# Kernel optimization log

Measured on AMD Instinct MI355X. Metric: run time of the kernel, lower is better.

## Reference

```python
import jax, jax.numpy as jnp
import numpy as np

P, C, D = 65536, 64, 256

def setup_inputs() -> dict:
    key = jax.random.key(0)
    k1, k2, k3, k4 = jax.random.split(key, 4)
    return {
        "protos1": jax.random.normal(k1, (P, D), dtype=jnp.float32),
        "protos2": jax.random.normal(k2, (P, D), dtype=jnp.float32),
        "W": jax.random.normal(k3, (D, D), dtype=jnp.float32) / np.float32(np.sqrt(D)),
        "b": jax.random.normal(k4, (D,), dtype=jnp.float32),
        "num_classes": C,
    }

def _pairwise_dist(x, y):
    # x: (C, n, D), y: (C, m, D) -> squared-euclidean-style dists (C, n, m)
    xs = jnp.sum(x * x, axis=-1)[:, :, None]
    ys = jnp.sum(y * y, axis=-1)[:, None, :]
    return xs + ys - 2.0 * jnp.einsum('cid,cjd->cij', x, y)

def reference(protos1, protos2, W, b, num_classes):
    nc = int(num_classes)
    d = protos1.shape[-1]
    # prototypes[c::num_classes] for all c at once: (P,D) -> (P//C, C, D) -> (C, P//C, D)
    p1 = protos1.reshape(-1, nc, d).transpose(1, 0, 2)
    p2 = protos2.reshape(-1, nc, d).transpose(1, 0, 2)
    # transition: nn.Linear -> x @ W.T + b ; inverse: (x - b) @ inv(W.T)
    p2_inv = (p2 - b) @ jnp.linalg.inv(W.T)
    p1_fwd = p1 @ W.T + b
    a = _pairwise_dist(p1, p2_inv)          # (C, n, n)
    bb = _pairwise_dist(p2, p1_fwd)         # (C, n, n)
    proto_losses_source = jnp.mean(jnp.min(a, axis=2), axis=1)   # (C,)
    proto_losses_target = jnp.mean(jnp.min(bb, axis=2), axis=1)  # (C,)
    return jnp.stack([proto_losses_source, proto_losses_target])  # (2, C)
```

## Files before the change

### kernel.cpp

```cpp
#include <hip/hip_runtime.h>

#define D 256
#define NC 64

using u16 = unsigned short;
using u32 = unsigned int;

typedef __attribute__((ext_vector_type(8))) short bfv8;
typedef __attribute__((ext_vector_type(4))) float f32x4;
typedef __attribute__((ext_vector_type(2))) int v2i;

__device__ __forceinline__ float bf2f(u32 u) {
  union { u32 i; float f; } v; v.i = u << 16; return v.f;
}
__device__ __forceinline__ u16 f2bf(float f) {
  union { float f; u32 i; } v; v.f = f;
  u32 x = v.i;
  return (u16)((x + 0x7FFFu + ((x >> 16) & 1u)) >> 16);
}
__device__ __forceinline__ u32 pk2(float a, float b) {
  return (u32)f2bf(a) | ((u32)f2bf(b) << 16);
}
__device__ __forceinline__ size_t cmrow(int g) {
  return (size_t)(((g & 63) << 10) | (g >> 6));
}

__device__ __forceinline__ void gload_lds16(const void* src, void* dst) {
  __builtin_amdgcn_global_load_lds(
      (const __attribute__((address_space(1))) void*)src,
      (__attribute__((address_space(3))) void*)dst, 16, 0, 0);
}

#define GJ_LDS 71168
#define DISTP_LDS 135680

__device__ void gj_body(const float* __restrict__ W, float* __restrict__ IW,
                        char* smem) {
  float (*Ml)[20]    = (float(*)[20])smem;
  float (*Arow)[256] = (float(*)[256])(smem + 20480);
  float (*G)[256]    = (float(*)[256])(smem + 36864);
  u16*  Gfrag        = (u16*)(smem + 53248);
  float (*Pinv)[20]  = (float(*)[20])(smem + 69888);
  const int t = threadIdx.x, w = t >> 6, l = t & 63;
  const int lj = l & 15, lh = l >> 4;
  const int r0 = 16 * w;
  const bool lo32 = (l < 32);

  f32x4 x[16];
#pragma unroll
  for (int ct = 0; ct < 16; ++ct)
#pragma unroll
    for (int reg = 0; reg < 4; ++reg)
      x[ct][reg] = W[(size_t)(r0 + 4 * lh + reg) * D + 16 * ct + lj];

  for (int s = 0; s < 16; ++s) {
#pragma unroll
    for (int ct = 0; ct < 16; ++ct)
      if (ct == s)
#pragma unroll
        for (int reg = 0; reg < 4; ++reg)
          Ml[r0 + 4 * lh + reg][lj] = x[ct][reg];
    if (w == s) {
#pragma unroll
      for (int ct = 0; ct < 16; ++ct)
#pragma unroll
        for (int reg = 0; reg < 4; ++reg)
          Arow[4 * lh + reg][16 * ct + lj] = x[ct][reg];
    }
    bfv8 afr;
    {
      const int row = r0 + lj;
      float4 f0 = *(const float4*)&Ml[row][8 * (lh & 1)];
      float4 f1 = *(const float4*)&Ml[row][8 * (lh & 1) + 4];
      const float fv[8] = {f0.x, f0.y, f0.z, f0.w, f1.x, f1.y, f1.z, f1.w};
      union { bfv8 v; u16 e[8]; } A;
      if (lh < 2) {
#pragma unroll
        for (int e = 0; e < 8; ++e) A.e[e] = f2bf(-fv[e]);
      } else {
#pragma unroll
        for (int e = 0; e < 8; ++e) {
          const float hi = bf2f(f2bf(fv[e]));
          A.e[e] = f2bf(-(fv[e] - hi));
        }
      }
      afr = A.v;
    }
    __syncthreads();
    if (t < 16) {
      float p[16];
      {
        float4 rr0 = *(const float4*)&Ml[16 * s + t][0];
        float4 rr1 = *(const float4*)&Ml[16 * s + t][4];
        float4 rr2 = *(const float4*)&Ml[16 * s + t][8];
        float4 rr3 = *(const float4*)&Ml[16 * s + t][12];
        p[0] = rr0.x; p[1] = rr0.y; p[2] = rr0.z; p[3] = rr0.w;
        p[4] = rr1.x; p[5] = rr1.y; p[6] = rr1.z; p[7] = rr1.w;
        p[8] = rr2.x; p[9] = rr2.y; p[10] = rr2.z; p[11] = rr2.w;
        p[12] = rr3.x; p[13] = rr3.y; p[14] = rr3.z; p[15] = rr3.w;
      }
#pragma unroll
      for (int pp = 0; pp < 16; ++pp) {
        float u[16];
#pragma unroll
        for (int j = 0; j < 16; ++j)
          u[j] = __int_as_float(__builtin_amdgcn_readlane(__float_as_int(p[j]), pp));
        const float pv = u[pp];
        const float d = 1.0f / pv;
        if (t == pp) {
#pragma unroll
          for (int j = 0; j < 16; ++j) p[j] = u[j] * d;
          p[pp] = d;
        } else {
          const float md = p[pp] * d;
          u[pp] = pv + 1.0f;
#pragma unroll
          for (int j = 0; j < 16; ++j) p[j] = fmaf(-md, u[j], p[j]);
        }
      }
#pragma unroll
      for (int j = 0; j < 16; ++j) Pinv[t][j] = p[j];
    }
    __syncthreads();
    {
      const bool inC = ((l >> 2) == s);
      const int co = (l & 3) << 2;
      const int gct = l >> 2;
      const int kk = w;
      float4 g = make_float4(0.f, 0.f, 0.f, 0.f);
#pragma unroll
      for (int q = 0; q < 16; ++q) {
        const float pv = Pinv[kk][q];
        const float4 av = *(const float4*)&Arow[q][4 * l];
        g.x = fmaf(pv, av.x, g.x); g.y = fmaf(pv, av.y, g.y);
        g.z = fmaf(pv, av.z, g.z); g.w = fmaf(pv, av.w, g.w);
      }
      if (inC) {
        g.x = Pinv[kk][co + 0] + (kk == co + 0 ? 1.f : 0.f);
        g.y = Pinv[kk][co + 1] + (kk == co + 1 ? 1.f : 0.f);
        g.z = Pinv[kk][co + 2] + (kk == co + 2 ? 1.f : 0.f);
        g.w = Pinv[kk][co + 3] + (kk == co + 3 ? 1.f : 0.f);
      }
      *(float4*)&G[kk][4 * l] = g;
      const int e0 = kk & 7;
      const int lbase = 16 * (kk >> 3);
      const float gv[4] = {g.x, g.y, g.z, g.w};
#pragma unroll
      for (int cc = 0; cc < 4; ++cc) {
        const int cl = 4 * (l & 3) + cc;
        const u16 hi = f2bf(gv[cc]);
        const u16 lo = f2bf(gv[cc] - bf2f(hi));
        Gfrag[gct * 520 + (lbase + cl) * 8 + e0] = hi;
        Gfrag[gct * 520 + (32 + lbase + cl) * 8 + e0] = lo;
      }
    }
    __syncthreads();
    if (w != s) {
#pragma unroll
      for (int ct = 0; ct < 16; ++ct) {
        union { bfv8 v; uint4 u; } B1, B2;
        B1.v = *(const bfv8*)&Gfrag[ct * 520 + l * 8];
#if __has_builtin(__builtin_amdgcn_permlane32_swap)
        {
          v2i r;
          r = __builtin_amdgcn_permlane32_swap((int)B1.u.x, (int)B1.u.x, false, false);
          B2.u.x = lo32 ? (u32)r.y : (u32)r.x;
          r = __builtin_amdgcn_permlane32_swap((int)B1.u.y, (int)B1.u.y, false, false);
          B2.u.y = lo32 ? (u32)r.y : (u32)r.x;
          r = __builtin_amdgcn_permlane32_swap((int)B1.u.z, (int)B1.u.z, false, false);
          B2.u.z = lo32 ? (u32)r.y : (u32)r.x;
          r = __builtin_amdgcn_permlane32_swap((int)B1.u.w, (int)B1.u.w, false, false);
          B2.u.w = lo32 ? (u32)r.y : (u32)r.x;
        }
#else
        B2.v = *(const bfv8*)&Gfrag[ct * 520 + (l ^ 32) * 8];
#endif
        x[ct] = __builtin_amdgcn_mfma_f32_16x16x32_bf16(afr, B1.v, x[ct], 0, 0, 0);
        x[ct] = __builtin_amdgcn_mfma_f32_16x16x32_bf16(afr, B2.v, x[ct], 0, 0, 0);
      }
    } else {
#pragma unroll
      for (int ct = 0; ct < 16; ++ct) {
        if (ct == s) {
#pragma unroll
          for (int reg = 0; reg < 4; ++reg)
            x[ct][reg] = Pinv[4 * lh + reg][lj];
        } else {
#pragma unroll
          for (int reg = 0; reg < 4; ++reg)
            x[ct][reg] = G[4 * lh + reg][16 * ct + lj];
        }
      }
    }
    __syncthreads();
  }
#pragma unroll
  for (int ct = 0; ct < 16; ++ct)
#pragma unroll
    for (int reg = 0; reg < 4; ++reg)
      IW[(size_t)(r0 + 4 * lh + reg) * D + 16 * ct + lj] = x[ct][reg];
}

__device__ void convnorm_role(const float* __restrict__ P, u16* __restrict__ Pb,
                              float* __restrict__ nrm, int blk) {
  const int tx = threadIdx.x;
  const int r = tx >> 2, q = tx & 3;
  const int g = blk * 256 + r;
  const float* src = P + (size_t)g * D + q * 64;
  u16* dst = Pb + cmrow(g) * D + q * 64;
  float ss = 0.f;
#pragma unroll
  for (int g4 = 0; g4 < 8; ++g4) {
    float4 v0 = *(const float4*)(src + g4 * 8);
    float4 v1 = *(const float4*)(src + g4 * 8 + 4);
    ss = fmaf(v0.x, v0.x, fmaf(v0.y, v0.y, fmaf(v0.z, v0.z, fmaf(v0.w, v0.w, ss))));
    ss = fmaf(v1.x, v1.x, fmaf(v1.y, v1.y, fmaf(v1.z, v1.z, fmaf(v1.w, v1.w, ss))));
    uint4 w4;
    w4.x = pk2(v0.x, v0.y); w4.y = pk2(v0.z, v0.w);
    w4.z = pk2(v1.x, v1.y); w4.w = pk2(v1.z, v1.w);
    *(uint4*)(dst + g4 * 8) = w4;
  }
  ss += __shfl_xor(ss, 1, 64);
  ss += __shfl_xor(ss, 2, 64);
  if (q == 0) nrm[cmrow(g)] = ss;
}

template <int MODE>
__device__ void distp_body(const float* __restrict__ Pj,
                           const u16* __restrict__ Brows,
                           const float* __restrict__ biasv,
                           const u16* __restrict__ Pib,
                           const float* __restrict__ nB,
                           float* __restrict__ pmind, int bid, char* smem) {
  const int lb = (bid & 7) * 64 + (bid >> 3);
  const int c = lb >> 3, jt = lb & 7;
  const int tx = threadIdx.x, ww = tx >> 6, l = tx & 63;
  const int mw = ww >> 3, nw = ww & 7, l4 = l >> 4, lm = l & 15;
  char* Ab = smem;
  char* Bb = smem + 65536;
  float* nfpart = (float*)(smem + 131072);
  float* minbuf = (float*)(smem + 131072);
  float* nAb = (float*)(smem + 135168);

  auto issue_chunk = [&](int buf, int ch) {
#pragma unroll
    for (int u = 0; u < 2; ++u) {
      const int chunk = ww * 2 + u, ks = chunk >> 2, n = chunk & 3;
      const u16* src = Pib + ((size_t)(c << 10) + ch * 64 + n * 16 + lm) * D
                       + ks * 32 + l4 * 8;
      gload_lds16(src, Bb + buf * 32768 + chunk * 1024);
    }
  };

  bfv8 bfr[2][8];
#pragma unroll
  for (int nf2 = 0; nf2 < 2; ++nf2)
#pragma unroll
    for (int ks = 0; ks < 8; ++ks)
      bfr[nf2][ks] = *(const bfv8*)(Brows +
          (size_t)(nw * 32 + nf2 * 16 + lm) * D + ks * 32 + l4 * 8);
  {
    const int r = tx >> 3, sg = tx & 7;
    const float* arow = Pj + ((size_t)(jt * 128 + r) * NC + c) * D + sg * 32;
#pragma unroll
    for (int g2 = 0; g2 < 4; ++g2) {
      float4 v0 = *(const float4*)(arow + g2 * 8);
      float4 v1 = *(const float4*)(arow + g2 * 8 + 4);
      uint4 w4;
      w4.x = pk2(v0.x, v0.y); w4.y = pk2(v0.z, v0.w);
      w4.z = pk2(v1.x, v1.y); w4.w = pk2(v1.z, v1.w);
      *(uint4*)(Ab + (sg * 8 + (r >> 4)) * 1024 + ((r & 15) + g2 * 16) * 16) = w4;
    }
  }
  __syncthreads();
  const bfv8* A8 = (const bfv8*)Ab;
  f32x4 acc[4][2];
#pragma unroll
  for (int mf = 0; mf < 4; ++mf) {
    acc[mf][0] = f32x4{0.f, 0.f, 0.f, 0.f};
    acc[mf][1] = f32x4{0.f, 0.f, 0.f, 0.f};
  }
#pragma unroll
  for (int ks = 0; ks < 8; ++ks)
#pragma unroll
    for (int mf = 0; mf < 4; ++mf) {
      bfv8 a = A8[(ks * 8 + mw * 4 + mf) * 64 + l];
      acc[mf][0] = __builtin_amdgcn_mfma_f32_16x16x32_bf16(a, bfr[0][ks], acc[mf][0], 0, 0, 0);
      acc[mf][1] = __builtin_amdgcn_mfma_f32_16x16x32_bf16(a, bfr[1][ks], acc[mf][1], 0, 0, 0);
    }
  float bias[2];
  if (MODE == 0) {
#pragma unroll
    for (int nf2 = 0; nf2 < 2; ++nf2)
      bias[nf2] = biasv[nw * 32 + nf2 * 16 + lm];
  } else {
#pragma unroll
    for (int nf2 = 0; nf2 < 2; ++nf2) {
      float pd = 0.f;
#pragma unroll
      for (int ks = 0; ks < 8; ++ks) {
        float4 b0 = *(const float4*)(biasv + ks * 32 + l4 * 8);
        float4 b1 = *(const float4*)(biasv + ks * 32 + l4 * 8 + 4);
        pd = fmaf(b0.x, bf2f((u16)bfr[nf2][ks][0]), pd);
        pd = fmaf(b0.y, bf2f((u16)bfr[nf2][ks][1]), pd);
        pd = fmaf(b0.z, bf2f((u16)bfr[nf2][ks][2]), pd);
        pd = fmaf(b0.w, bf2f((u16)bfr[nf2][ks][3]), pd);
        pd = fmaf(b1.x, bf2f((u16)bfr[nf2][ks][4]), pd);
        pd = fmaf(b1.y, bf2f((u16)bfr[nf2][ks][5]), pd);
        pd = fmaf(b1.z, bf2f((u16)bfr[nf2][ks][6]), pd);
        pd = fmaf(b1.w, bf2f((u16)bfr[nf2][ks][7]), pd);
      }
      pd += __shfl_xor(pd, 16, 64);
      pd += __shfl_xor(pd, 32, 64);
      bias[nf2] = -pd;
    }
  }
  __syncthreads();
  issue_chunk(0, 0);
  u16* tile = (u16*)Ab;
#pragma unroll
  for (int mf = 0; mf < 4; ++mf)
#pragma unroll
    for (int rr = 0; rr < 4; ++rr) {
      const int j = mw * 64 + mf * 16 + l4 * 4 + rr;
      float v2 = 0.f;
#pragma unroll
      for (int nf2 = 0; nf2 < 2; ++nf2) {
        const float v = acc[mf][nf2][rr] + bias[nf2];
        const u16 hv = f2bf(v);
        tile[(((nw * 8 + mw * 4 + mf) << 6) + ((nf2 * 2 + (lm >> 3)) << 4)
              + l4 * 4 + rr) * 8 + (lm & 7)] = hv;
        const float vr = bf2f(hv);
        v2 = fmaf(vr, vr, v2);
      }
      v2 += __shfl_xor(v2, 1, 64);
      v2 += __shfl_xor(v2, 2, 64);
      v2 += __shfl_xor(v2, 4, 64);
      v2 += __shfl_xor(v2, 8, 64);
      if (lm == 0) nfpart[nw * 128 + j] = v2;
    }
  __syncthreads();
  if (tx < 128) {
    float s = 0.f;
#pragma unroll
    for (int q = 0; q < 8; ++q) s += nfpart[q * 128 + tx];
    nAb[tx] = s;
  }
  __syncthreads();
  const int jw = ww >> 1, iw = ww & 1;
  const float* nBc = nB + (c << 10);
  const size_t obase = (size_t)(c * 8 + jt) * 1024;
  for (int ch = 0; ch < 16; ++ch) {
    if (ch < 15) issue_chunk((ch + 1) & 1, ch + 1);
    const bfv8* B8 = (const bfv8*)(Bb + (ch & 1) * 32768);
    f32x4 a2[2];
    a2[0] = f32x4{0.f, 0.f, 0.f, 0.f};
    a2[1] = f32x4{0.f, 0.f, 0.f, 0.f};
#pragma unroll
    for (int ks = 0; ks < 8; ++ks) {
      bfv8 a = A8[(ks * 8 + jw) * 64 + l];
#pragma unroll
      for (int t = 0; t < 2; ++t) {
        bfv8 b = B8[(ks * 4 + iw * 2 + t) * 64 + l];
        a2[t] = __builtin_amdgcn_mfma_f32_16x16x32_bf16(a, b, a2[t], 0, 0, 0);
      }
    }
#pragma unroll
    for (int t = 0; t < 2; ++t) {
      const int ig = iw * 2 + t;
      const float nb = nBc[ch * 64 + ig * 16 + lm];
      float mm = 3.0e38f;
#pragma unroll
      for (int rr = 0; rr < 4; ++rr) {
        const int j = jw * 16 + l4 * 4 + rr;
        const float dd = nb + nAb[j] - 2.0f * a2[t][rr];
        mm = fminf(mm, dd);
      }
      mm = fminf(mm, __shfl_xor(mm, 16, 64));
      mm = fminf(mm, __shfl_xor(mm, 32, 64));
      if (l4 == 0) minbuf[jw * 64 + ig * 16 + lm] = mm;
    }
    __syncthreads();
    if (tx < 64) {
      float m = minbuf[tx];
#pragma unroll
      for (int q = 1; q < 8; ++q) m = fminf(m, minbuf[q * 64 + tx]);
      pmind[obase + ch * 64 + tx] = m;
    }
    __syncthreads();
  }
}

__global__ __launch_bounds__(1024, 1) void k0_kernel(
    const float* __restrict__ p2, u16* __restrict__ p2b,
    float* __restrict__ n2, const float* __restrict__ W,
    u16* __restrict__ Wb) {
  if (blockIdx.x < 256) {
    convnorm_role(p2, p2b, n2, blockIdx.x);
  } else {
    const int t = threadIdx.x;
#pragma unroll
    for (int k = 0; k < 64; ++k) Wb[k * 1024 + t] = f2bf(W[k * 1024 + t]);
  }
}

__global__ __launch_bounds__(1024, 1) void k1_kernel(
    const float* __restrict__ p1, const float* __restrict__ W,
    const u16* __restrict__ Wb, const float* __restrict__ bv,
    const u16* __restrict__ p2b, const float* __restrict__ n2,
    float* __restrict__ pmin1, float* __restrict__ IWa,
    u16* __restrict__ p1b, float* __restrict__ n1) {
  extern __shared__ char smem[];
  const int b = blockIdx.x;
  if (b == 0) {
    gj_body(W, IWa, smem);
  } else if (b <= 512) {
    distp_body<0>(p1, Wb, bv, p2b, n2, pmin1, b - 1, smem);
  } else {
    convnorm_role(p1, p1b, n1, b - 513);
  }
}

__global__ __launch_bounds__(256) void nr_residual(const float* __restrict__ W,
                                                   const float* __restrict__ X,
                                                   float* __restrict__ R) {
  __shared__ float wrow[D];
  const int i = blockIdx.x, j = threadIdx.x;
  wrow[j] = W[i * D + j];
  __syncthreads();
  float acc = 0.f;
#pragma unroll 8
  for (int k = 0; k < D; ++k) acc = fmaf(wrow[k], X[k * D + j], acc);
  R[i * D + j] = (i == j ? 2.0f : 0.0f) - acc;
}

__global__ __launch_bounds__(256) void nr_mult_bf16(const float* __restrict__ X,
                                                    const float* __restrict__ R,
                                                    u16* __restrict__ Yb) {
  __shared__ float xrow[D];
  const int i = blockIdx.x, j = threadIdx.x;
  xrow[j] = X[i * D + j];
  __syncthreads();
  float acc = 0.f;
#pragma unroll 8
  for (int k = 0; k < D; ++k) acc = fmaf(xrow[k], R[k * D + j], acc);
  Yb[i * D + j] = f2bf(acc);
}

__global__ __launch_bounds__(1024, 1) void k3_kernel(
    const float* __restrict__ p2, const u16* __restrict__ IWb,
    const float* __restrict__ bv, const u16* __restrict__ p1b,
    const float* __restrict__ n1, float* __restrict__ pmin0) {
  extern __shared__ char smem[];
  distp_body<1>(p2, IWb, bv, p1b, n1, pmin0, blockIdx.x, smem);
}

__global__ __launch_bounds__(256) void final_kernel(const float* __restrict__ pmin,
                                                    float* __restrict__ out) {
  __shared__ float ws4[4];
  const int dc = blockIdx.x, tx = threadIdx.x;
  const float* base = pmin + (size_t)dc * 8192;
  float s = 0.f;
#pragma unroll
  for (int t = 0; t < 4; ++t) {
    const int i = t * 256 + tx;
    float m = base[i];
#pragma unroll
    for (int j = 1; j < 8; ++j) m = fminf(m, base[j * 1024 + i]);
    s += m;
  }
#pragma unroll
  for (int off = 32; off; off >>= 1) s += __shfl_xor(s, off, 64);
  if ((tx & 63) == 0) ws4[tx >> 6] = s;
  __syncthreads();
  if (tx == 0)
    out[dc] = (ws4[0] + ws4[1] + ws4[2] + ws4[3]) * (1.0f / 1024.0f);
}

extern "C" void kernel_launch(void* const* d_in, const int* in_sizes, int n_in,
                              void* d_out, int out_size, void* d_ws, size_t ws_size,
                              hipStream_t stream) {
  const float* p1 = (const float*)d_in[0];
  const float* p2 = (const float*)d_in[1];
  const float* W  = (const float*)d_in[2];
  const float* bv = (const float*)d_in[3];
  float* out = (float*)d_out;
  char* ws = (char*)d_ws;
  float* n1  = (float*)(ws);
  float* n2  = (float*)(ws + (256 << 10));
  u16* Wb    = (u16*)(ws + (512 << 10));
  u16* IWb   = (u16*)(ws + (640 << 10));
  float* IWa = (float*)(ws + (768 << 10));
  float* Rt  = (float*)(ws + (1024 << 10));
  float* pmin = (float*)(ws + (1280 << 10));
  u16* p1b   = (u16*)(ws + (6u << 20));
  u16* p2b   = (u16*)(ws + (38u << 20));
  float* pmin0 = pmin;
  float* pmin1 = pmin + 524288;

  hipFuncSetAttribute((const void*)k1_kernel,
                      hipFuncAttributeMaxDynamicSharedMemorySize, DISTP_LDS);
  hipFuncSetAttribute((const void*)k3_kernel,
                      hipFuncAttributeMaxDynamicSharedMemorySize, DISTP_LDS);

  k0_kernel<<<257, 1024, 0, stream>>>(p2, p2b, n2, W, Wb);
  k1_kernel<<<769, 1024, DISTP_LDS, stream>>>(p1, W, Wb, bv, p2b, n2,
                                              pmin1, IWa, p1b, n1);
  nr_residual<<<256, 256, 0, stream>>>(W, IWa, Rt);
  nr_mult_bf16<<<256, 256, 0, stream>>>(IWa, Rt, IWb);
  k3_kernel<<<512, 1024, DISTP_LDS, stream>>>(p2, IWb, bv, p1b, n1, pmin0);
  final_kernel<<<128, 256, 0, stream>>>(pmin, out);
}
```

Baseline: 281.9 us.

## Hold A fragments in registers and reuse A tile LDS for B double buffer

Each wave now loads its two 16-row A fragments from LDS into registers once, then reuses the A tile region as the double buffer for streamed B chunks. Dynamic LDS for the distance kernels drops from about 135KB to about 70KB. The wave-to-tile mapping is also changed so each wave computes two row tiles against one column tile, which halves B fragment LDS reads and the min-reduction width. Costs are higher register pressure from the 16 held bfv8 fragments, an extra barrier, and the first B prefetch now being issued later.

Measured after the change: 279.0 us. About the same (-1.0%).

```diff
diff --git a/kernel.cpp b/kernel.cpp
--- a/kernel.cpp
+++ b/kernel.cpp
@@ -31,8 +31,8 @@
       (__attribute__((address_space(3))) void*)dst, 16, 0, 0);
 }
 
-#define GJ_LDS 71168
-#define DISTP_LDS 135680
+#define K1_LDS 71168
+#define DISTP_LDS 70144
 
 __device__ void gj_body(const float* __restrict__ W, float* __restrict__ IW,
                         char* smem) {
@@ -237,10 +237,9 @@
   const int tx = threadIdx.x, ww = tx >> 6, l = tx & 63;
   const int mw = ww >> 3, nw = ww & 7, l4 = l >> 4, lm = l & 15;
   char* Ab = smem;
-  char* Bb = smem + 65536;
-  float* nfpart = (float*)(smem + 131072);
-  float* minbuf = (float*)(smem + 131072);
-  float* nAb = (float*)(smem + 135168);
+  float* nfpart = (float*)(smem + 65536);
+  float* minbuf = (float*)(smem + 65536);
+  float* nAb = (float*)(smem + 69632);
 
   auto issue_chunk = [&](int buf, int ch) {
 #pragma unroll
@@ -248,7 +247,7 @@
       const int chunk = ww * 2 + u, ks = chunk >> 2, n = chunk & 3;
       const u16* src = Pib + ((size_t)(c << 10) + ch * 64 + n * 16 + lm) * D
                        + ks * 32 + l4 * 8;
-      gload_lds16(src, Bb + buf * 32768 + chunk * 1024);
+      gload_lds16(src, Ab + buf * 32768 + chunk * 1024);
     }
   };
 
@@ -316,7 +315,6 @@
     }
   }
   __syncthreads();
-  issue_chunk(0, 0);
   u16* tile = (u16*)Ab;
 #pragma unroll
   for (int mf = 0; mf < 4; ++mf)
@@ -340,6 +338,15 @@
       if (lm == 0) nfpart[nw * 128 + j] = v2;
     }
   __syncthreads();
+  const int jw = ww >> 2, iw = ww & 3;
+  bfv8 afr[2][8];
+#pragma unroll
+  for (int jj = 0; jj < 2; ++jj)
+#pragma unroll
+    for (int ks = 0; ks < 8; ++ks)
+      afr[jj][ks] = A8[(ks * 8 + jw * 2 + jj) * 64 + l];
+  __syncthreads();
+  issue_chunk(0, 0);
   if (tx < 128) {
     float s = 0.f;
 #pragma unroll
@@ -347,44 +354,43 @@
     nAb[tx] = s;
   }
   __syncthreads();
-  const int jw = ww >> 1, iw = ww & 1;
+  float naj[2][4];
+#pragma unroll
+  for (int jj = 0; jj < 2; ++jj)
+#pragma unroll
+    for (int rr = 0; rr < 4; ++rr)
+      naj[jj][rr] = nAb[jw * 32 + jj * 16 + l4 * 4 + rr];
   const float* nBc = nB + (c << 10);
   const size_t obase = (size_t)(c * 8 + jt) * 1024;
   for (int ch = 0; ch < 16; ++ch) {
     if (ch < 15) issue_chunk((ch + 1) & 1, ch + 1);
-    const bfv8* B8 = (const bfv8*)(Bb + (ch & 1) * 32768);
+    const bfv8* B8 = (const bfv8*)(Ab + (ch & 1) * 32768);
     f32x4 a2[2];
     a2[0] = f32x4{0.f, 0.f, 0.f, 0.f};
     a2[1] = f32x4{0.f, 0.f, 0.f, 0.f};
 #pragma unroll
     for (int ks = 0; ks < 8; ++ks) {
-      bfv8 a = A8[(ks * 8 + jw) * 64 + l];
-#pragma unroll
-      for (int t = 0; t < 2; ++t) {
-        bfv8 b = B8[(ks * 4 + iw * 2 + t) * 64 + l];
-        a2[t] = __builtin_amdgcn_mfma_f32_16x16x32_bf16(a, b, a2[t], 0, 0, 0);
-      }
-    }
-#pragma unroll
-    for (int t = 0; t < 2; ++t) {
-      const int ig = iw * 2 + t;
-      const float nb = nBc[ch * 64 + ig * 16 + lm];
-      float mm = 3.0e38f;
+      bfv8 b = B8[(ks * 4 + iw) * 64 + l];
+      a2[0] = __builtin_amdgcn_mfma_f32_16x16x32_bf16(afr[0][ks], b, a2[0], 0, 0, 0);
+      a2[1] = __builtin_amdgcn_mfma_f32_16x16x32_bf16(afr[1][ks], b, a2[1], 0, 0, 0);
+    }
+    const float nb = nBc[ch * 64 + iw * 16 + lm];
+    float mm = 3.0e38f;
+#pragma unroll
+    for (int jj = 0; jj < 2; ++jj)
 #pragma unroll
       for (int rr = 0; rr < 4; ++rr) {
-        const int j = jw * 16 + l4 * 4 + rr;
-        const float dd = nb + nAb[j] - 2.0f * a2[t][rr];
+        const float dd = nb + naj[jj][rr] - 2.0f * a2[jj][rr];
         mm = fminf(mm, dd);
       }
-      mm = fminf(mm, __shfl_xor(mm, 16, 64));
-      mm = fminf(mm, __shfl_xor(mm, 32, 64));
-      if (l4 == 0) minbuf[jw * 64 + ig * 16 + lm] = mm;
-    }
+    mm = fminf(mm, __shfl_xor(mm, 16, 64));
+    mm = fminf(mm, __shfl_xor(mm, 32, 64));
+    if (l4 == 0) minbuf[jw * 64 + iw * 16 + lm] = mm;
     __syncthreads();
     if (tx < 64) {
       float m = minbuf[tx];
 #pragma unroll
-      for (int q = 1; q < 8; ++q) m = fminf(m, minbuf[q * 64 + tx]);
+      for (int q = 1; q < 4; ++q) m = fminf(m, minbuf[q * 64 + tx]);
       pmind[obase + ch * 64 + tx] = m;
     }
     __syncthreads();
@@ -499,13 +505,13 @@
   float* pmin1 = pmin + 524288;
 
   hipFuncSetAttribute((const void*)k1_kernel,
-                      hipFuncAttributeMaxDynamicSharedMemorySize, DISTP_LDS);
+                      hipFuncAttributeMaxDynamicSharedMemorySize, K1_LDS);
   hipFuncSetAttribute((const void*)k3_kernel,
                       hipFuncAttributeMaxDynamicSharedMemorySize, DISTP_LDS);
 
   k0_kernel<<<257, 1024, 0, stream>>>(p2, p2b, n2, W, Wb);
-  k1_kernel<<<769, 1024, DISTP_LDS, stream>>>(p1, W, Wb, bv, p2b, n2,
-                                              pmin1, IWa, p1b, n1);
+  k1_kernel<<<769, 1024, K1_LDS, stream>>>(p1, W, Wb, bv, p2b, n2,
+                                           pmin1, IWa, p1b, n1);
   nr_residual<<<256, 256, 0, stream>>>(W, IWa, Rt);
   nr_mult_bf16<<<256, 256, 0, stream>>>(IWa, Rt, IWb);
   k3_kernel<<<512, 1024, DISTP_LDS, stream>>>(p2, IWb, bv, p1b, n1, pmin0);
```
